# Performance work log

Measured on AMD Instinct MI355X. Metric: run time of the kernel, lower is better.

Reference implementation:

```python
import jax, jax.numpy as jnp
import numpy as np
import math

H = 512
B = 32
S = 4096

def setup_inputs() -> dict:
    key = jax.random.key(0)
    ks = jax.random.split(key, 7)
    bound = 1.0 / math.sqrt(H)
    query = jax.random.normal(ks[0], (B, H), dtype=jnp.float32)
    ref = jax.random.normal(ks[1], (B, S, H), dtype=jnp.float32)
    # nn.Linear(H, H): weight [H, H], bias [H]
    Wq = jax.random.uniform(ks[2], (H, H), minval=-bound, maxval=bound, dtype=jnp.float32)
    bq = jax.random.uniform(ks[3], (H,), minval=-bound, maxval=bound, dtype=jnp.float32)
    # nn.Conv1d(H, H, 1): weight [H, H, 1] -> squeeze to [H, H], bias [H]
    Wr = jax.random.uniform(ks[4], (H, H), minval=-bound, maxval=bound, dtype=jnp.float32)
    br = jax.random.uniform(ks[5], (H,), minval=-bound, maxval=bound, dtype=jnp.float32)
    V = jax.random.uniform(ks[6], (H,), minval=-bound, maxval=bound, dtype=jnp.float32)
    return {"query": query, "ref": ref, "Wq": Wq, "bq": bq, "Wr": Wr, "br": br, "V": V}

def reference(query, ref, Wq, bq, Wr, br, V):
    # q_proj: [B, H]; Linear applies x @ W.T + b
    q = query @ Wq.T + bq
    # Conv1d with kernel 1 over channels == per-position linear: [B, S, H]
    r = jnp.einsum('bsh,oh->bso', ref, Wr) + br
    # additive score: V . tanh(q + r) over hidden dim -> [B, S]
    logits = jnp.einsum('bsh,h->bs', jnp.tanh(q[:, None, :] + r), V)
    weights = jax.nn.softmax(logits, axis=1)
    # expected annotation over PROJECTED ref (as in original): [B, H, 1]
    out = jnp.einsum('bsh,bs->bh', r, weights)[:, :, None]
    return out
```

## Files before the change

kernel.cpp:

```cpp
#include <hip/hip_runtime.h>
#include <hip/hip_bf16.h>

#define HDIM 512
#define BB 32
#define SS 4096
#define TR 64
#define NCH (SS/TR)
#define NBLK (BB*NCH)

typedef __attribute__((ext_vector_type(8))) short short8;
typedef __attribute__((ext_vector_type(4))) float f32x4;

#define WS_QB    0
#define WS_WRBF  65536
#define WS_PM    (65536+524288)
#define WS_PD    (WS_PM+16384)
#define WS_PU    (WS_PD+16384)

__device__ __forceinline__ unsigned cvt_pk_bf16(float lo, float hi){
  unsigned r;
  asm("v_cvt_pk_bf16_f32 %0, %1, %2" : "=v"(r) : "v"(lo), "v"(hi));
  return r;
}

__global__ __launch_bounds__(256) void k_prep(const float* __restrict__ Wr,
                                              unsigned short* __restrict__ wrbF,
                                              const float* __restrict__ query,
                                              const float* __restrict__ Wq,
                                              const float* __restrict__ bq,
                                              const float* __restrict__ br,
                                              float* __restrict__ qb){
  int t = threadIdx.x;
  if (blockIdx.x < 128){
    int gid = blockIdx.x*256 + t;
    int lane = gid & 63;
    int tile = gid >> 6;
    int kt = tile & 15, t16 = tile >> 4;
    int col = t16*16 + (lane & 15);
    int k0  = kt*32 + (lane >> 4)*8;
    const float* src = Wr + (size_t)col*HDIM + k0;
    f32x4 v0 = *(const f32x4*)(src);
    f32x4 v1 = *(const f32x4*)(src + 4);
    uint4 o;
    o.x = cvt_pk_bf16(v0.x, v0.y);
    o.y = cvt_pk_bf16(v0.z, v0.w);
    o.z = cvt_pk_bf16(v1.x, v1.y);
    o.w = cvt_pk_bf16(v1.z, v1.w);
    *(uint4*)(wrbF + (size_t)gid*8) = o;
  } else {
    __shared__ __align__(16) float sq[HDIM];
    int b = blockIdx.x - 128;
    sq[t] = query[b*HDIM + t];
    sq[t+256] = query[b*HDIM + t + 256];
    __syncthreads();
    const f32x4* sq4 = (const f32x4*)sq;
    for (int hh = 0; hh < 2; ++hh){
      int h = t + hh*256;
      const f32x4* w4 = (const f32x4*)(Wq + (size_t)h*HDIM);
      float acc = bq[h] + br[h];
      #pragma unroll 4
      for (int k = 0; k < HDIM/4; ++k){
        f32x4 w = w4[k]; f32x4 q = sq4[k];
        acc += w.x*q.x + w.y*q.y + w.z*q.z + w.w*q.w;
      }
      qb[b*HDIM + h] = acc;
    }
  }
}

__global__ __launch_bounds__(512)
__attribute__((amdgpu_waves_per_eu(4, 4)))
void k_main(const float* __restrict__ ref,
            const unsigned short* __restrict__ wrbF,
            const float* __restrict__ qb,
            const float* __restrict__ V,
            float* __restrict__ pm,
            float* __restrict__ pd,
            float* __restrict__ pu){
  int bid = blockIdx.x;
  int b = bid >> 6;
  int chunk = bid & 63;
  int tid = threadIdx.x;
  int w = tid >> 6, lane = tid & 63;
  int lo16 = lane & 15, g = lane >> 4;

  __shared__ __align__(16) unsigned short sA[TR*HDIM];
  __shared__ __align__(16) float sQb[HDIM];
  __shared__ __align__(16) float sV[HDIM];
  __shared__ float sLog[8][TR];
  __shared__ float sE[TR];
  __shared__ __align__(16) float sUa[2][HDIM];

  sQb[tid] = qb[b*HDIM + tid];
  sV[tid]  = V[tid];

  {
    const f32x4* s4 = (const f32x4*)(ref + ((size_t)b*SS + (size_t)chunk*TR)*HDIM) + tid;
    #pragma unroll
    for (int p = 0; p < 2; ++p){
      f32x4 R[8];
      #pragma unroll
      for (int i = 0; i < 8; ++i) R[i] = s4[p*4096 + 512*i];
      #pragma unroll
      for (int i = 0; i < 8; ++i){
        int idx = tid + 512*i + p*4096;
        int row = idx >> 7, c4 = idx & 127;
        f32x4 v = R[i];
        uint2 o;
        o.x = cvt_pk_bf16(v.x, v.y);
        o.y = cvt_pk_bf16(v.z, v.w);
        unsigned byte = (unsigned)(row*1024) + (((unsigned)c4*8) ^ ((unsigned)(row & 7) << 4));
        *(uint2*)((char*)sA + byte) = o;
      }
    }
  }
  __syncthreads();

  const float C2L2E = 2.8853900817779268f;
  float lacc[4][4];
  #pragma unroll
  for (int m = 0; m < 4; ++m)
    #pragma unroll
    for (int r = 0; r < 4; ++r)
      lacc[m][r] = 0.f;
  float SV = 0.f;

  #pragma unroll
  for (int nh = 0; nh < 2; ++nh){
    int tbase = w*4 + nh*2;
    const short8* wfp = (const short8*)wrbF + ((size_t)tbase*16*64 + lane);
    f32x4 acc[4][2];
    #pragma unroll
    for (int m = 0; m < 4; ++m)
      #pragma unroll
      for (int n = 0; n < 2; ++n)
        acc[m][n] = (f32x4){0.f, 0.f, 0.f, 0.f};

    #pragma unroll 4
    for (int kt = 0; kt < 16; ++kt){
      short8 af[4];
      #pragma unroll
      for (int m = 0; m < 4; ++m){
        int row = 16*m + lo16;
        unsigned byte = (unsigned)(row*1024) + (((unsigned)(kt*64 + g*16)) ^ ((unsigned)(row & 7) << 4));
        af[m] = *(const short8*)((const char*)sA + byte);
      }
      short8 bfr[2];
      bfr[0] = wfp[kt*64];
      bfr[1] = wfp[1024 + kt*64];
      #pragma unroll
      for (int m = 0; m < 4; ++m)
        #pragma unroll
        for (int n = 0; n < 2; ++n)
          acc[m][n] = __builtin_amdgcn_mfma_f32_16x16x32_bf16(af[m], bfr[n], acc[m][n], 0, 0, 0);
    }

    #pragma unroll
    for (int n = 0; n < 2; ++n){
      int col = (tbase + n)*16 + lo16;
      float qc  = C2L2E * sQb[col];
      float vv  = sV[col];
      float vv2 = -2.f * vv;
      SV += vv;
      #pragma unroll
      for (int m = 0; m < 4; ++m)
        #pragma unroll
        for (int r = 0; r < 4; ++r){
          float e  = __builtin_amdgcn_exp2f(__builtin_fmaf(C2L2E, acc[m][n][r], qc));
          float rc = __builtin_amdgcn_rcpf(1.f + e);
          lacc[m][r] = __builtin_fmaf(vv2, rc, lacc[m][r]);
        }
    }
  }
  #pragma unroll
  for (int m = 0; m < 4; ++m)
    #pragma unroll
    for (int r = 0; r < 4; ++r)
      lacc[m][r] += SV;

  #pragma unroll
  for (int m = 0; m < 4; ++m)
    #pragma unroll
    for (int r = 0; r < 4; ++r){
      float v = lacc[m][r];
      v += __shfl_xor(v, 1); v += __shfl_xor(v, 2);
      v += __shfl_xor(v, 4); v += __shfl_xor(v, 8);
      lacc[m][r] = v;
    }
  if (lo16 == 0){
    #pragma unroll
    for (int m = 0; m < 4; ++m)
      #pragma unroll
      for (int r = 0; r < 4; ++r)
        sLog[w][16*m + 4*g + r] = lacc[m][r];
  }
  __syncthreads();

  if (w == 0){
    float l = sLog[0][lane] + sLog[1][lane] + sLog[2][lane] + sLog[3][lane]
            + sLog[4][lane] + sLog[5][lane] + sLog[6][lane] + sLog[7][lane];
    float mx = l;
    mx = fmaxf(mx, __shfl_xor(mx, 1));  mx = fmaxf(mx, __shfl_xor(mx, 2));
    mx = fmaxf(mx, __shfl_xor(mx, 4));  mx = fmaxf(mx, __shfl_xor(mx, 8));
    mx = fmaxf(mx, __shfl_xor(mx, 16)); mx = fmaxf(mx, __shfl_xor(mx, 32));
    float e = __expf(l - mx);
    float d = e;
    d += __shfl_xor(d, 1); d += __shfl_xor(d, 2); d += __shfl_xor(d, 4);
    d += __shfl_xor(d, 8); d += __shfl_xor(d, 16); d += __shfl_xor(d, 32);
    sE[lane] = e;
    if (lane == 0){ pm[bid] = mx; pd[bid] = d; }
  }
  __syncthreads();

  {
    int h = tid >> 8, t8 = tid & 255;
    const char* sAB = (const char*)sA + (unsigned)h*32768u;
    const float* eh = sE + h*32;
    float u0 = 0.f, u1 = 0.f;
    #pragma unroll 8
    for (int s2 = 0; s2 < 32; ++s2){
      unsigned byte = (unsigned)(s2*1024) + (((unsigned)(t8*4)) ^ ((unsigned)(s2 & 7) << 4));
      unsigned pk = *(const unsigned*)(sAB + byte);
      float e = eh[s2];
      u0 += e * __uint_as_float((pk & 0xFFFFu) << 16);
      u1 += e * __uint_as_float(pk & 0xFFFF0000u);
    }
    sUa[h][2*t8]     = u0;
    sUa[h][2*t8 + 1] = u1;
  }
  __syncthreads();
  pu[(size_t)bid*HDIM + tid] = sUa[0][tid] + sUa[1][tid];
}

__global__ __launch_bounds__(256) void k_final(const float* __restrict__ Wr,
                                               const float* __restrict__ br,
                                               const float* __restrict__ pm,
                                               const float* __restrict__ pd,
                                               const float* __restrict__ pu,
                                               float* __restrict__ out){
  int b = blockIdx.x, t = threadIdx.x, lane = t & 63, w = t >> 6;
  __shared__ float sSc[NCH];
  __shared__ __align__(16) float sU[HDIM];
  __shared__ float sMD0;

  if (w == 0){
    float m = pm[b*NCH + lane];
    float mx = m;
    mx = fmaxf(mx, __shfl_xor(mx, 1));  mx = fmaxf(mx, __shfl_xor(mx, 2));
    mx = fmaxf(mx, __shfl_xor(mx, 4));  mx = fmaxf(mx, __shfl_xor(mx, 8));
    mx = fmaxf(mx, __shfl_xor(mx, 16)); mx = fmaxf(mx, __shfl_xor(mx, 32));
    float sc = __expf(m - mx);
    float d = sc * pd[b*NCH + lane];
    d += __shfl_xor(d, 1); d += __shfl_xor(d, 2); d += __shfl_xor(d, 4);
    d += __shfl_xor(d, 8); d += __shfl_xor(d, 16); d += __shfl_xor(d, 32);
    sSc[lane] = sc;
    if (lane == 0) sMD0 = d;
  }
  __syncthreads();

  float inv = 1.f / sMD0;
  float u0 = 0.f, u1 = 0.f;
  for (int c = 0; c < NCH; ++c){
    float sc = sSc[c];
    const float* p = pu + ((size_t)(b*NCH + c))*HDIM;
    u0 += sc * p[t];
    u1 += sc * p[t+256];
  }
  sU[t]     = u0 * inv;
  sU[t+256] = u1 * inv;
  __syncthreads();

  const f32x4* su4 = (const f32x4*)sU;
  for (int hh = 0; hh < 2; ++hh){
    int h = t + hh*256;
    const f32x4* w4 = (const f32x4*)(Wr + (size_t)h*HDIM);
    float acc = br[h];
    #pragma unroll 4
    for (int k = 0; k < HDIM/4; ++k){
      f32x4 wv = w4[k], uv = su4[k];
      acc += wv.x*uv.x + wv.y*uv.y + wv.z*uv.z + wv.w*uv.w;
    }
    out[b*HDIM + h] = acc;
  }
}

extern "C" void kernel_launch(void* const* d_in, const int* in_sizes, int n_in,
                              void* d_out, int out_size, void* d_ws, size_t ws_size,
                              hipStream_t stream){
  const float* query = (const float*)d_in[0];
  const float* ref   = (const float*)d_in[1];
  const float* Wq    = (const float*)d_in[2];
  const float* bq    = (const float*)d_in[3];
  const float* Wr    = (const float*)d_in[4];
  const float* br    = (const float*)d_in[5];
  const float* V     = (const float*)d_in[6];
  char* ws = (char*)d_ws;
  float*          qbv  = (float*)(ws + WS_QB);
  unsigned short* wrbF = (unsigned short*)(ws + WS_WRBF);
  float*          pm   = (float*)(ws + WS_PM);
  float*          pd   = (float*)(ws + WS_PD);
  float*          pu   = (float*)(ws + WS_PU);
  float* out = (float*)d_out;

  k_prep<<<dim3(160), dim3(256), 0, stream>>>(Wr, wrbF, query, Wq, bq, br, qbv);
  k_main<<<dim3(NBLK), dim3(512), 0, stream>>>(ref, wrbF, qbv, V, pm, pd, pu);
  k_final<<<dim3(BB), dim3(256), 0, stream>>>(Wr, br, pm, pd, pu, out);
}
```

Baseline: 169.5 us.

## Reuse MFMA projection accumulators for weighted sum, drop final Wr GEMV

The main kernel now keeps all 16 MFMA accumulator tiles (4x4) live across the whole K loop instead of two passes of 4x2. It then forms the softmax-weighted sum directly on the projected values r (not on raw ref), which removes the LDS re-read pass, the sUa buffer and one barrier. Because the weighted sum is already in projected space, the final kernel no longer does a per-batch 512x512 Wr matrix-vector product and just adds the bias. It also simplifies the swizzled LDS address math. In exchange it needs more live registers (64 accumulator floats per lane) under a 4-waves-per-EU bound, which risks spilling, and it makes the output depend on bf16-rounded accumulator values.

```diff
diff --git a/kernel.cpp b/kernel.cpp
--- a/kernel.cpp
+++ b/kernel.cpp
@@ -15,7 +15,7 @@
 #define WS_WRBF  65536
 #define WS_PM    (65536+524288)
 #define WS_PD    (WS_PM+16384)
-#define WS_PU    (WS_PD+16384)
+#define WS_PRB   (WS_PD+16384)
 
 __device__ __forceinline__ unsigned cvt_pk_bf16(float lo, float hi){
   unsigned r;
@@ -76,7 +76,7 @@
             const float* __restrict__ V,
             float* __restrict__ pm,
             float* __restrict__ pd,
-            float* __restrict__ pu){
+            float* __restrict__ prb){
   int bid = blockIdx.x;
   int b = bid >> 6;
   int chunk = bid & 63;
@@ -88,8 +88,7 @@
   __shared__ __align__(16) float sQb[HDIM];
   __shared__ __align__(16) float sV[HDIM];
   __shared__ float sLog[8][TR];
-  __shared__ float sE[TR];
-  __shared__ __align__(16) float sUa[2][HDIM];
+  __shared__ __align__(16) float sE[TR];
 
   sQb[tid] = qb[b*HDIM + tid];
   sV[tid]  = V[tid];
@@ -116,6 +115,40 @@
   }
   __syncthreads();
 
+  unsigned baseA = (unsigned)(lo16*1024) + (((unsigned)g*16) ^ ((unsigned)(lo16 & 3) << 4));
+  unsigned bsel  = (unsigned)((lo16 >> 2) & 1) * 64u;
+  const char* pAe = (const char*)sA + baseA + bsel;
+  const char* pAo = (const char*)sA + baseA - bsel + 64;
+  const short8* wfp = (const short8*)wrbF + ((size_t)(w*4)*16*64 + lane);
+
+  f32x4 acc[4][4];
+  #pragma unroll
+  for (int m = 0; m < 4; ++m)
+    #pragma unroll
+    for (int n = 0; n < 4; ++n)
+      acc[m][n] = (f32x4){0.f, 0.f, 0.f, 0.f};
+
+  #pragma unroll 4
+  for (int kt = 0; kt < 16; ++kt){
+    short8 af[4];
+    #pragma unroll
+    for (int m = 0; m < 4; ++m){
+      if (kt & 1)
+        af[m] = *(const short8*)(pAo + (m*16384 + (kt-1)*64));
+      else
+        af[m] = *(const short8*)(pAe + (m*16384 + kt*64));
+    }
+    short8 bfr[4];
+    #pragma unroll
+    for (int n = 0; n < 4; ++n)
+      bfr[n] = wfp[(size_t)n*1024 + kt*64];
+    #pragma unroll
+    for (int m = 0; m < 4; ++m)
+      #pragma unroll
+      for (int n = 0; n < 4; ++n)
+        acc[m][n] = __builtin_amdgcn_mfma_f32_16x16x32_bf16(af[m], bfr[n], acc[m][n], 0, 0, 0);
+  }
+
   const float C2L2E = 2.8853900817779268f;
   float lacc[4][4];
   #pragma unroll
@@ -126,51 +159,20 @@
   float SV = 0.f;
 
   #pragma unroll
-  for (int nh = 0; nh < 2; ++nh){
-    int tbase = w*4 + nh*2;
-    const short8* wfp = (const short8*)wrbF + ((size_t)tbase*16*64 + lane);
-    f32x4 acc[4][2];
-    #pragma unroll
-    for (int m = 0; m < 4; ++m)
-      #pragma unroll
-      for (int n = 0; n < 2; ++n)
-        acc[m][n] = (f32x4){0.f, 0.f, 0.f, 0.f};
-
-    #pragma unroll 4
-    for (int kt = 0; kt < 16; ++kt){
-      short8 af[4];
-      #pragma unroll
-      for (int m = 0; m < 4; ++m){
-        int row = 16*m + lo16;
-        unsigned byte = (unsigned)(row*1024) + (((unsigned)(kt*64 + g*16)) ^ ((unsigned)(row & 7) << 4));
-        af[m] = *(const short8*)((const char*)sA + byte);
+  for (int n = 0; n < 4; ++n){
+    int col = w*64 + n*16 + lo16;
+    float qc  = C2L2E * sQb[col];
+    float vv  = sV[col];
+    float vv2 = -2.f * vv;
+    SV += vv;
+    #pragma unroll
+    for (int m = 0; m < 4; ++m)
+      #pragma unroll
+      for (int r = 0; r < 4; ++r){
+        float e  = __builtin_amdgcn_exp2f(__builtin_fmaf(C2L2E, acc[m][n][r], qc));
+        float rc = __builtin_amdgcn_rcpf(1.f + e);
+        lacc[m][r] = __builtin_fmaf(vv2, rc, lacc[m][r]);
       }
-      short8 bfr[2];
-      bfr[0] = wfp[kt*64];
-      bfr[1] = wfp[1024 + kt*64];
-      #pragma unroll
-      for (int m = 0; m < 4; ++m)
-        #pragma unroll
-        for (int n = 0; n < 2; ++n)
-          acc[m][n] = __builtin_amdgcn_mfma_f32_16x16x32_bf16(af[m], bfr[n], acc[m][n], 0, 0, 0);
-    }
-
-    #pragma unroll
-    for (int n = 0; n < 2; ++n){
-      int col = (tbase + n)*16 + lo16;
-      float qc  = C2L2E * sQb[col];
-      float vv  = sV[col];
-      float vv2 = -2.f * vv;
-      SV += vv;
-      #pragma unroll
-      for (int m = 0; m < 4; ++m)
-        #pragma unroll
-        for (int r = 0; r < 4; ++r){
-          float e  = __builtin_amdgcn_exp2f(__builtin_fmaf(C2L2E, acc[m][n][r], qc));
-          float rc = __builtin_amdgcn_rcpf(1.f + e);
-          lacc[m][r] = __builtin_fmaf(vv2, rc, lacc[m][r]);
-        }
-    }
   }
   #pragma unroll
   for (int m = 0; m < 4; ++m)
@@ -213,34 +215,33 @@
   __syncthreads();
 
   {
-    int h = tid >> 8, t8 = tid & 255;
-    const char* sAB = (const char*)sA + (unsigned)h*32768u;
-    const float* eh = sE + h*32;
-    float u0 = 0.f, u1 = 0.f;
-    #pragma unroll 8
-    for (int s2 = 0; s2 < 32; ++s2){
-      unsigned byte = (unsigned)(s2*1024) + (((unsigned)(t8*4)) ^ ((unsigned)(s2 & 7) << 4));
-      unsigned pk = *(const unsigned*)(sAB + byte);
-      float e = eh[s2];
-      u0 += e * __uint_as_float((pk & 0xFFFFu) << 16);
-      u1 += e * __uint_as_float(pk & 0xFFFF0000u);
-    }
-    sUa[h][2*t8]     = u0;
-    sUa[h][2*t8 + 1] = u1;
-  }
-  __syncthreads();
-  pu[(size_t)bid*HDIM + tid] = sUa[0][tid] + sUa[1][tid];
-}
-
-__global__ __launch_bounds__(256) void k_final(const float* __restrict__ Wr,
-                                               const float* __restrict__ br,
+    f32x4 e4[4];
+    #pragma unroll
+    for (int m = 0; m < 4; ++m)
+      e4[m] = *(const f32x4*)&sE[16*m + 4*g];
+    #pragma unroll
+    for (int n = 0; n < 4; ++n){
+      float rb = 0.f;
+      #pragma unroll
+      for (int m = 0; m < 4; ++m)
+        #pragma unroll
+        for (int r = 0; r < 4; ++r)
+          rb = __builtin_fmaf(e4[m][r], acc[m][n][r], rb);
+      rb += __shfl_xor(rb, 16);
+      rb += __shfl_xor(rb, 32);
+      if (g == 0)
+        prb[(size_t)bid*HDIM + w*64 + n*16 + lo16] = rb;
+    }
+  }
+}
+
+__global__ __launch_bounds__(256) void k_final(const float* __restrict__ br,
                                                const float* __restrict__ pm,
                                                const float* __restrict__ pd,
-                                               const float* __restrict__ pu,
+                                               const float* __restrict__ prb,
                                                float* __restrict__ out){
   int b = blockIdx.x, t = threadIdx.x, lane = t & 63, w = t >> 6;
   __shared__ float sSc[NCH];
-  __shared__ __align__(16) float sU[HDIM];
   __shared__ float sMD0;
 
   if (w == 0){
@@ -262,26 +263,12 @@
   float u0 = 0.f, u1 = 0.f;
   for (int c = 0; c < NCH; ++c){
     float sc = sSc[c];
-    const float* p = pu + ((size_t)(b*NCH + c))*HDIM;
+    const float* p = prb + ((size_t)(b*NCH + c))*HDIM;
     u0 += sc * p[t];
     u1 += sc * p[t+256];
   }
-  sU[t]     = u0 * inv;
-  sU[t+256] = u1 * inv;
-  __syncthreads();
-
-  const f32x4* su4 = (const f32x4*)sU;
-  for (int hh = 0; hh < 2; ++hh){
-    int h = t + hh*256;
-    const f32x4* w4 = (const f32x4*)(Wr + (size_t)h*HDIM);
-    float acc = br[h];
-    #pragma unroll 4
-    for (int k = 0; k < HDIM/4; ++k){
-      f32x4 wv = w4[k], uv = su4[k];
-      acc += wv.x*uv.x + wv.y*uv.y + wv.z*uv.z + wv.w*uv.w;
-    }
-    out[b*HDIM + h] = acc;
-  }
+  out[b*HDIM + t]       = u0 * inv + br[t];
+  out[b*HDIM + t + 256] = u1 * inv + br[t + 256];
 }
 
 extern "C" void kernel_launch(void* const* d_in, const int* in_sizes, int n_in,
@@ -299,10 +286,10 @@
   unsigned short* wrbF = (unsigned short*)(ws + WS_WRBF);
   float*          pm   = (float*)(ws + WS_PM);
   float*          pd   = (float*)(ws + WS_PD);
-  float*          pu   = (float*)(ws + WS_PU);
+  float*          prb  = (float*)(ws + WS_PRB);
   float* out = (float*)d_out;
 
   k_prep<<<dim3(160), dim3(256), 0, stream>>>(Wr, wrbF, query, Wq, bq, br, qbv);
-  k_main<<<dim3(NBLK), dim3(512), 0, stream>>>(ref, wrbF, qbv, V, pm, pd, pu);
-  k_final<<<dim3(BB), dim3(256), 0, stream>>>(Wr, br, pm, pd, pu, out);
-}
+  k_main<<<dim3(NBLK), dim3(512), 0, stream>>>(ref, wrbF, qbv, V, pm, pd, prb);
+  k_final<<<dim3(BB), dim3(256), 0, stream>>>(br, pm, pd, prb, out);
+}
```

Result: faster. 136.7 us, median of 3 (-19.4%).
